# Performance work log

Hardware: AMD Instinct MI355X
Metric: run time of the kernel (lower is better)

## Reference

```python
import jax, jax.numpy as jnp
import numpy as np

EPS = 1e-5

def _conv2d(x, w, b, pad):
    # NCHW conv, stride 1
    out = jax.lax.conv_general_dilated(x, w, (1, 1), [(pad, pad), (pad, pad)],
                                       dimension_numbers=('NCHW', 'OIHW', 'NCHW'))
    return out + b[None, :, None, None]

def _deform_conv2d(x, offset, mask, weight, bias, pad):
    # torchvision.ops.deform_conv2d (modulated, stride=1, dilation=1)
    B, C, H, W = x.shape
    O, _, K, _ = weight.shape
    kk = K * K
    off = offset.reshape(B, kk, 2, H, W)
    dy, dx = off[:, :, 0], off[:, :, 1]          # [B,kk,H,W]
    ki = (jnp.arange(kk) // K).astype(x.dtype)
    kj = (jnp.arange(kk) % K).astype(x.dtype)
    hh = jnp.arange(H, dtype=x.dtype)
    ww = jnp.arange(W, dtype=x.dtype)
    ys = dy + (hh[None, :, None] + ki[:, None, None] - pad)[None]  # [B,kk,H,W]
    xs = dx + (ww[None, None, :] + kj[:, None, None] - pad)[None]
    y0 = jnp.floor(ys); x0 = jnp.floor(xs)
    wy = ys - y0; wx = xs - x0
    xf = x.reshape(B, C, H * W)

    def gather(yi, xi):
        valid = ((yi >= 0) & (yi <= H - 1) & (xi >= 0) & (xi <= W - 1)).astype(x.dtype)
        yc = jnp.clip(yi, 0, H - 1).astype(jnp.int32)
        xc = jnp.clip(xi, 0, W - 1).astype(jnp.int32)
        idx = (yc * W + xc).reshape(B, -1)
        v = jax.vmap(lambda f, i: f[:, i])(xf, idx).reshape(B, C, kk, H, W)
        return v * valid[:, None]

    one = jnp.asarray(1.0, x.dtype)
    sampled = (gather(y0, x0) * ((one - wy) * (one - wx))[:, None]
               + gather(y0, x0 + 1) * ((one - wy) * wx)[:, None]
               + gather(y0 + 1, x0) * (wy * (one - wx))[:, None]
               + gather(y0 + 1, x0 + 1) * (wy * wx)[:, None])
    sampled = sampled * mask[:, None]            # modulation
    out = jnp.einsum('bckhw,ock->bohw', sampled, weight.reshape(O, C, kk))
    return out + bias[None, :, None, None]

def setup_inputs() -> dict:
    key = jax.random.key(0)
    ks = jax.random.split(key, 7)
    B, C, H, W = 8, 768, 32, 32
    x = jax.random.normal(ks[0], (B, C, H, W), jnp.float32)
    proj_w = jax.random.normal(ks[1], (768, 768, 3, 3), jnp.float32) * 0.02
    proj_b = jax.random.normal(ks[2], (768,), jnp.float32) * 0.02
    offset_w = jax.random.normal(ks[3], (18, 768, 3, 3), jnp.float32) * 0.01
    offset_b = jax.random.normal(ks[4], (18,), jnp.float32) * 0.01
    mask_w = jax.random.normal(ks[5], (9, 768, 3, 3), jnp.float32) * 0.01
    mask_b = jax.random.normal(ks[6], (9,), jnp.float32) * 0.01
    gamma = jnp.ones((768,), jnp.float32)
    beta = jnp.zeros((768,), jnp.float32)
    return {"x": x, "proj_w": proj_w, "proj_b": proj_b, "offset_w": offset_w,
            "offset_b": offset_b, "mask_w": mask_w, "mask_b": mask_b,
            "gamma": gamma, "beta": beta}

def reference(x, proj_w, proj_b, offset_w, offset_b, mask_w, mask_b, gamma, beta):
    pad = 1
    H, W = x.shape[-2], x.shape[-1]
    max_off = float(min(H, W) // 4)
    offset = jnp.clip(_conv2d(x, offset_w, offset_b, pad), -max_off, max_off)
    mask = 2.0 * jax.nn.sigmoid(_conv2d(x, mask_w, mask_b, pad))
    y = _deform_conv2d(x, offset, mask, proj_w, proj_b, pad)
    # SyncBatchNorm (training-mode batch statistics, biased var)
    mean = jnp.mean(y, axis=(0, 2, 3))
    var = jnp.var(y, axis=(0, 2, 3))
    yn = (y - mean[None, :, None, None]) * jax.lax.rsqrt(var + EPS)[None, :, None, None]
    yn = yn * gamma[None, :, None, None] + beta[None, :, None, None]
    return x + jax.nn.gelu(yn, approximate=False)
```

## Files before the change

### kernel.cpp

```cpp
#include <hip/hip_runtime.h>
#include <math.h>

typedef __attribute__((ext_vector_type(4))) float f32x4;
typedef __attribute__((ext_vector_type(8))) short s16x8;
typedef __attribute__((ext_vector_type(4))) unsigned int u32x4;
typedef unsigned short ushort_t;

#define HW   1024
#define C_IN 768
#define B_N  8

__device__ inline ushort_t f2bf(float f) {
    unsigned u = __builtin_bit_cast(unsigned, f);
    unsigned r = u + 0x7FFFu + ((u >> 16) & 1u);
    return (ushort_t)(r >> 16);
}
__device__ inline float bf2f(short s) {
    return __builtin_bit_cast(float, ((unsigned)(ushort_t)s) << 16);
}
__device__ inline void glds16(const void* g, void* l) {
    __builtin_amdgcn_global_load_lds(
        (const __attribute__((address_space(1))) unsigned*)g,
        (__attribute__((address_space(3))) unsigned*)l, 16, 0, 0);
}

__global__ __launch_bounds__(256) void prepack_xt(
    const float* __restrict__ x, ushort_t* __restrict__ xt)
{
    __shared__ ushort_t tile[64][66];
    int bid = blockIdx.x;
    int b  = bid / 192;
    int r  = bid % 192;
    int cg = r / 16, pg = r % 16;
    int c0 = cg * 64, p0 = pg * 64;
    int t = threadIdx.x;
#pragma unroll
    for (int i = 0; i < 16; ++i) {
        int idx = t + i * 256;
        int cr = idx >> 6, col = idx & 63;
        tile[cr][col] = f2bf(x[(((size_t)b * C_IN + c0 + cr) << 10) + p0 + col]);
    }
    __syncthreads();
#pragma unroll
    for (int i = 0; i < 16; ++i) {
        int idx = t + i * 256;
        int pr = idx >> 6, col = idx & 63;
        xt[((size_t)(b << 10) + p0 + pr) * C_IN + c0 + col] = tile[col][pr];
    }
}

__global__ __launch_bounds__(256) void prepack_proj(
    const float* __restrict__ pw, ushort_t* __restrict__ A)
{
    __shared__ ushort_t tile[16][584];
    int bid = blockIdx.x;
    int mf = bid / 12, cblk = bid - mf * 12;
    int t = threadIdx.x;
    const float* src = pw + (size_t)mf * 16 * 6912 + cblk * 576;
#pragma unroll
    for (int i = 0; i < 36; ++i) {
        int f = i * 256 + t;
        int orow = f / 576, col = f - orow * 576;
        tile[orow][col] = f2bf(src[(size_t)orow * 6912 + col]);
    }
    __syncthreads();
    int lane = t & 63, fi0 = t >> 6;
    for (int it = 0; it < 5; ++it) {
        int fidx = it * 4 + fi0;
        if (fidx < 18) {
            int tap = fidx >> 1, half = fidx & 1;
            int s = tap * 24 + cblk * 2 + half;
            int cl0 = half * 32 + ((lane >> 4) << 3);
            s16x8 pk;
#pragma unroll
            for (int e = 0; e < 8; ++e)
                pk[e] = (short)tile[lane & 15][(cl0 + e) * 9 + tap];
            *(s16x8*)(A + ((size_t)(s * 48 + mf) * 64 + lane) * 8) = pk;
        }
    }
}

__global__ __launch_bounds__(256) void prepack_om(
    const float* __restrict__ offw, const float* __restrict__ mskw,
    ushort_t* __restrict__ A2)
{
    int t = blockIdx.x * 256 + threadIdx.x;
    int lane = t & 63;
    int smi  = t >> 6;
    int s  = smi >> 1, mf = smi & 1;
    int oc = mf * 16 + (lane & 15);
    int k0 = s * 32 + ((lane >> 4) << 3);
    int tap = k0 / 768;
    int c   = k0 - tap * 768;
    s16x8 pk;
#pragma unroll
    for (int e = 0; e < 8; ++e) pk[e] = 0;
    if (oc < 27) {
        const float* src = (oc < 18)
            ? offw + ((size_t)oc        * 768 + c) * 9 + tap
            : mskw + ((size_t)(oc - 18) * 768 + c) * 9 + tap;
#pragma unroll
        for (int e = 0; e < 8; ++e) pk[e] = (short)f2bf(src[e * 9]);
    }
    *(s16x8*)(A2 + (size_t)smi * 512 + lane * 8) = pk;
}

__global__ __launch_bounds__(256) void offmask_mfma(
    const ushort_t* __restrict__ xt, const ushort_t* __restrict__ A2,
    const float* __restrict__ offb, const float* __restrict__ mbias,
    float* __restrict__ offs, float* __restrict__ maskb)
{
    int bid = blockIdx.x;
    int b = bid >> 5, pt = bid & 31;
    int p0 = pt << 5;
    int t = threadIdx.x, lane = t & 63, wv = t >> 6;
    int mf = wv >> 1, nf = wv & 1;
    int q = lane >> 4;
    int px = p0 + nf * 16 + (lane & 15);
    int h = px >> 5, w = px & 31;
    const char* xb = (const char*)xt + (size_t)b * (HW * 1536);
    f32x4 acc = (f32x4){0.f, 0.f, 0.f, 0.f};

    for (int tap = 0; tap < 9; ++tap) {
        int yy = h + tap / 3 - 1, xx = w + tap % 3 - 1;
        bool ok = (yy >= 0 && yy < 32 && xx >= 0 && xx < 32);
        int pos = ok ? (yy * 32 + xx) : 0;
        const char* bp = xb + (size_t)pos * 1536 + q * 16;
        for (int cs = 0; cs < 24; ++cs) {
            int s = tap * 24 + cs;
            s16x8 bf;
            if (ok) bf = *(const s16x8*)(bp + cs * 64);
            else    bf = (s16x8){0, 0, 0, 0, 0, 0, 0, 0};
            s16x8 af = *(const s16x8*)(A2 + ((size_t)(s * 2 + mf) * 64 + lane) * 8);
            acc = __builtin_amdgcn_mfma_f32_16x16x32_bf16(af, bf, acc, 0, 0, 0);
        }
    }
#pragma unroll
    for (int r = 0; r < 4; ++r) {
        int oc = mf * 16 + ((lane >> 4) << 2) + r;
        if (oc < 18) {
            float v = acc[r] + offb[oc];
            v = fminf(fmaxf(v, -8.f), 8.f);
            offs[((b * 18 + oc) << 10) + px] = v;
        } else if (oc < 27) {
            float v = acc[r] + mbias[oc - 18];
            maskb[((b * 9 + oc - 18) << 10) + px] = 2.f / (1.f + expf(-v));
        }
    }
}

__global__ __launch_bounds__(512) void sample_pack(
    const ushort_t* __restrict__ xt,
    const float* __restrict__ offs, const float* __restrict__ maskb,
    ushort_t* __restrict__ Bp)
{
    __shared__ float4 mw[9][16];
    __shared__ int4   mi[9][16];
    int bid = blockIdx.x;
    int b = bid >> 6, pxg = bid & 63;
    int px0 = pxg << 4;
    int t = threadIdx.x;

    if (t < 144) {
        int tap = t >> 4, pxl = t & 15;
        int px = px0 + pxl, h = px >> 5, w = px & 31;
        float dy = offs[((b * 18 + 2 * tap) << 10) + px];
        float dx = offs[((b * 18 + 2 * tap + 1) << 10) + px];
        float m  = maskb[((b * 9 + tap) << 10) + px];
        float ys = dy + (float)(h + tap / 3 - 1);
        float xs = dx + (float)(w + tap % 3 - 1);
        float fy = floorf(ys), fx = floorf(xs);
        float wy = ys - fy, wx = xs - fx;
        int iy0 = (int)fy, ix0 = (int)fx;
        int iy1 = iy0 + 1, ix1 = ix0 + 1;
        float vy0 = (iy0 >= 0 && iy0 < 32) ? 1.f : 0.f;
        float vy1 = (iy1 >= 0 && iy1 < 32) ? 1.f : 0.f;
        float vx0 = (ix0 >= 0 && ix0 < 32) ? 1.f : 0.f;
        float vx1 = (ix1 >= 0 && ix1 < 32) ? 1.f : 0.f;
        int cy0 = min(max(iy0, 0), 31), cx0 = min(max(ix0, 0), 31);
        int cy1 = min(max(iy1, 0), 31), cx1 = min(max(ix1, 0), 31);
        float4 wv4;
        wv4.x = (1.f - wy) * (1.f - wx) * m * vy0 * vx0;
        wv4.y = (1.f - wy) * wx         * m * vy0 * vx1;
        wv4.z = wy         * (1.f - wx) * m * vy1 * vx0;
        wv4.w = wy         * wx         * m * vy1 * vx1;
        mw[tap][pxl] = wv4;
        mi[tap][pxl] = make_int4((cy0 * 32 + cx0) * 1536, (cy0 * 32 + cx1) * 1536,
                                 (cy1 * 32 + cx0) * 1536, (cy1 * 32 + cx1) * 1536);
    }
    __syncthreads();

    int lane = t & 63, wv = t >> 6;
    int pxl = lane & 15, ko = lane >> 4;
    const char* xb = (const char*)xt + (size_t)b * (HW * 1536);

    for (int s = wv; s < 216; s += 8) {
        int tap = s / 24, cq = s - tap * 24;
        float4 w4 = mw[tap][pxl];
        int4  i4 = mi[tap][pxl];
        const char* base = xb + cq * 64 + ko * 16;
        s16x8 g0 = *(const s16x8*)(base + i4.x);
        s16x8 g1 = *(const s16x8*)(base + i4.y);
        s16x8 g2 = *(const s16x8*)(base + i4.z);
        s16x8 g3 = *(const s16x8*)(base + i4.w);
        u32x4 bw;
#pragma unroll
        for (int e2 = 0; e2 < 4; ++e2) {
            float v0 = w4.x * bf2f(g0[2 * e2])     + w4.y * bf2f(g1[2 * e2])
                     + w4.z * bf2f(g2[2 * e2])     + w4.w * bf2f(g3[2 * e2]);
            float v1 = w4.x * bf2f(g0[2 * e2 + 1]) + w4.y * bf2f(g1[2 * e2 + 1])
                     + w4.z * bf2f(g2[2 * e2 + 1]) + w4.w * bf2f(g3[2 * e2 + 1]);
            unsigned rr;
            asm("v_cvt_pk_bf16_f32 %0, %1, %2" : "=v"(rr) : "v"(v0), "v"(v1));
            bw[e2] = rr;
        }
        *(u32x4*)(Bp + ((size_t)(s * 8 + b) * 64 + pxg) * 512 + lane * 8) = bw;
    }
}

__global__ __launch_bounds__(512, 4) void deform_gemm_lds(
    const ushort_t* __restrict__ Amat, const ushort_t* __restrict__ Bp,
    float* __restrict__ y)
{
    __shared__ __align__(16) char Sbuf[2][32768];

    int id = blockIdx.x;
    int b = id & 7;
    int pxt = (id >> 3) & 15;
    int otile = id >> 7;
    int p0 = pxt << 6;
    int t = threadIdx.x, lane = t & 63, wv = t >> 6;
    int wm = wv >> 1, wn = wv & 1;

    f32x4 acc[3][2];
#pragma unroll
    for (int f = 0; f < 3; ++f)
#pragma unroll
        for (int n = 0; n < 2; ++n) acc[f][n] = (f32x4){0.f, 0.f, 0.f, 0.f};

#define STAGE(BUF, P) do {                                                  \
    int s0_ = 2 * (P);                                                      \
    _Pragma("unroll")                                                       \
    for (int i_ = 0; i_ < 4; ++i_) {                                        \
        int c_ = wv * 4 + i_;                                               \
        const char* src_;                                                   \
        if (c_ < 24) {                                                      \
            int kk_ = c_ / 12, f_ = c_ - kk_ * 12;                          \
            src_ = (const char*)Amat +                                      \
                (((size_t)(s0_ + kk_) * 48 + otile * 12 + f_) << 10);       \
        } else {                                                            \
            int d_ = c_ - 24; int kk_ = d_ >> 2, pg_ = d_ & 3;              \
            src_ = (const char*)Bp +                                        \
                (((size_t)((s0_ + kk_) * 8 + b) * 64 + pxt * 4 + pg_) << 10); \
        }                                                                   \
        glds16(src_ + lane * 16, &Sbuf[BUF][c_ << 10]);                     \
    }                                                                       \
} while (0)

#define MFMA_PHASE(BUF) do {                                                \
    _Pragma("unroll")                                                       \
    for (int kk_ = 0; kk_ < 2; ++kk_) {                                     \
        const char* ab_ = &Sbuf[BUF][(kk_ * 12 + wm * 3) << 10] + lane * 16; \
        s16x8 a0_ = *(const s16x8*)(ab_);                                   \
        s16x8 a1_ = *(const s16x8*)(ab_ + 1024);                            \
        s16x8 a2_ = *(const s16x8*)(ab_ + 2048);                            \
        const char* bb_ = &Sbuf[BUF][(24 + kk_ * 4 + wn * 2) << 10] + lane * 16; \
        s16x8 b0_ = *(const s16x8*)(bb_);                                   \
        s16x8 b1_ = *(const s16x8*)(bb_ + 1024);                            \
        acc[0][0] = __builtin_amdgcn_mfma_f32_16x16x32_bf16(a0_, b0_, acc[0][0], 0, 0, 0); \
        acc[0][1] = __builtin_amdgcn_mfma_f32_16x16x32_bf16(a0_, b1_, acc[0][1], 0, 0, 0); \
        acc[1][0] = __builtin_amdgcn_mfma_f32_16x16x32_bf16(a1_, b0_, acc[1][0], 0, 0, 0); \
        acc[1][1] = __builtin_amdgcn_mfma_f32_16x16x32_bf16(a1_, b1_, acc[1][1], 0, 0, 0); \
        acc[2][0] = __builtin_amdgcn_mfma_f32_16x16x32_bf16(a2_, b0_, acc[2][0], 0, 0, 0); \
        acc[2][1] = __builtin_amdgcn_mfma_f32_16x16x32_bf16(a2_, b1_, acc[2][1], 0, 0, 0); \
    }                                                                       \
} while (0)

    STAGE(0, 0);
    asm volatile("s_waitcnt vmcnt(0)" ::: "memory");
    __builtin_amdgcn_s_barrier();

    for (int p = 0; p < 108; ++p) {
        int buf = p & 1;
        if (p + 1 < 108) STAGE(buf ^ 1, p + 1);
        __builtin_amdgcn_s_setprio(1);
        MFMA_PHASE(buf);
        __builtin_amdgcn_s_setprio(0);
        asm volatile("s_waitcnt vmcnt(0) lgkmcnt(0)" ::: "memory");
        __builtin_amdgcn_s_barrier();
    }

    int pxo = p0 + wn * 32 + (lane & 15);
    int obase = otile * 192 + wm * 48;
#pragma unroll
    for (int f = 0; f < 3; ++f) {
        int orow = obase + f * 16 + ((lane >> 4) << 2);
#pragma unroll
        for (int r = 0; r < 4; ++r) {
            size_t rowoff = ((size_t)(b * 768 + orow + r) << 10);
            y[rowoff + pxo]      = acc[f][0][r];
            y[rowoff + pxo + 16] = acc[f][1][r];
        }
    }
#undef STAGE
#undef MFMA_PHASE
}

__global__ __launch_bounds__(512, 4) void deform_mfma_fused(
    const ushort_t* __restrict__ xt, const ushort_t* __restrict__ Amat,
    const float* __restrict__ offs, const float* __restrict__ maskb,
    float* __restrict__ y)
{
    __shared__ float4 meta_w[576];
    __shared__ int4   meta_i[576];
    __shared__ __align__(16) ushort_t Bs[2][64][64];

    int id = blockIdx.x;
    int b = id & 7;
    int pxt = (id >> 3) & 15;
    int otile = id >> 7;
    int p0 = pxt << 6;
    int t = threadIdx.x, lane = t & 63, wv = t >> 6;
    int wm = wv >> 1, wn = wv & 1;
    int q4 = lane >> 4;

    int bpx = wv * 8 + (lane >> 3);
    int oct = lane & 7;
    const int wchunk = (oct ^ (bpx & 7)) * 8;

    for (int i = t; i < 576; i += 512) {
        int k = i >> 6, j = i & 63;
        int hw = p0 + j, h = hw >> 5, w = hw & 31;
        float dy = offs[((b * 18 + 2 * k) << 10) + hw];
        float dx = offs[((b * 18 + 2 * k + 1) << 10) + hw];
        float m  = maskb[((b * 9 + k) << 10) + hw];
        float ys = dy + (float)(h + k / 3 - 1);
        float xs = dx + (float)(w + k % 3 - 1);
        float fy = floorf(ys), fx = floorf(xs);
        float wy = ys - fy, wx = xs - fx;
        int iy0 = (int)fy, ix0 = (int)fx;
        int iy1 = iy0 + 1, ix1 = ix0 + 1;
        float vy0 = (iy0 >= 0 && iy0 < 32) ? 1.f : 0.f;
        float vy1 = (iy1 >= 0 && iy1 < 32) ? 1.f : 0.f;
        float vx0 = (ix0 >= 0 && ix0 < 32) ? 1.f : 0.f;
        float vx1 = (ix1 >= 0 && ix1 < 32) ? 1.f : 0.f;
        int cy0 = min(max(iy0, 0), 31), cx0 = min(max(ix0, 0), 31);
        int cy1 = min(max(iy1, 0), 31), cx1 = min(max(ix1, 0), 31);
        float4 wv4;
        wv4.x = (1.f - wy) * (1.f - wx) * m * vy0 * vx0;
        wv4.y = (1.f - wy) * wx         * m * vy0 * vx1;
        wv4.z = wy         * (1.f - wx) * m * vy1 * vx0;
        wv4.w = wy         * wx         * m * vy1 * vx1;
        meta_w[i] = wv4;
        meta_i[i] = make_int4((cy0 * 32 + cx0) * 1536, (cy0 * 32 + cx1) * 1536,
                              (cy1 * 32 + cx0) * 1536, (cy1 * 32 + cx1) * 1536);
    }
    asm volatile("s_waitcnt lgkmcnt(0)" ::: "memory");
    __builtin_amdgcn_s_barrier();

    f32x4 acc[3][2];
#pragma unroll
    for (int f = 0; f < 3; ++f)
#pragma unroll
        for (int n = 0; n < 2; ++n) acc[f][n] = (f32x4){0.f, 0.f, 0.f, 0.f};

    const char* xb = (const char*)xt + (size_t)b * (HW * 1536);
    const int afrag0 = otile * 12 + wm * 3;

    s16x8 ga0, ga1, ga2, ga3, gb0, gb1, gb2, gb3;
    float4 w4a, w4b;

#define WBAR() do { asm volatile("s_waitcnt lgkmcnt(0)" ::: "memory"); \
                    __builtin_amdgcn_s_barrier(); } while (0)
#define ISSUE(G0, G1, G2, G3, W4, qq) do {                                  \
    int nt_ = (qq) / 12, nc_ = (qq) - nt_ * 12;                             \
    W4 = meta_w[nt_ * 64 + bpx];                                            \
    int4 i4_ = meta_i[nt_ * 64 + bpx];                                      \
    const char* bsrc_ = xb + nc_ * 128 + oct * 16;                          \
    G0 = *(const s16x8*)(bsrc_ + i4_.x);                                    \
    G1 = *(const s16x8*)(bsrc_ + i4_.y);                                    \
    G2 = *(const s16x8*)(bsrc_ + i4_.z);                                    \
    G3 = *(const s16x8*)(bsrc_ + i4_.w);                                    \
} while (0)
#define BUILD(G0, G1, G2, G3, W4, BUF) do {                                 \
    u32x4 bw_;                                                              \
    _Pragma("unroll")                                                       \
    for (int e2 = 0; e2 < 4; ++e2) {                                        \
        float v0_ = W4.x * bf2f(G0[2*e2])   + W4.y * bf2f(G1[2*e2])         \
                  + W4.z * bf2f(G2[2*e2])   + W4.w * bf2f(G3[2*e2]);        \
        float v1_ = W4.x * bf2f(G0[2*e2+1]) + W4.y * bf2f(G1[2*e2+1])       \
                  + W4.z * bf2f(G2[2*e2+1]) + W4.w * bf2f(G3[2*e2+1]);      \
        unsigned rr_;                                                       \
        asm("v_cvt_pk_bf16_f32 %0, %1, %2" : "=v"(rr_) : "v"(v0_), "v"(v1_)); \
        bw_[e2] = rr_;                                                      \
    }                                                                       \
    *(u32x4*)&Bs[BUF][bpx][wchunk] = bw_;                                   \
} while (0)
#define MFMA_PHASE_F(P, BUF) do {                                           \
    _Pragma("unroll")                                                       \
    for (int kk = 0; kk < 2; ++kk) {                                        \
        int s_ = 2 * (P) + kk;                                              \
        const s16x8* ap_ = (const s16x8*)(Amat +                            \
            ((size_t)(s_ * 48 + afrag0) * 64 + lane) * 8);                  \
        s16x8 a0_ = ap_[0], a1_ = ap_[64], a2_ = ap_[128];                  \
        int rc_ = ((kk * 4 + q4) ^ (lane & 7)) * 8;                         \
        s16x8 b0_ = *(const s16x8*)&Bs[BUF][wn * 32 + (lane & 15)][rc_];    \
        s16x8 b1_ = *(const s16x8*)&Bs[BUF][wn * 32 + 16 + (lane & 15)][rc_]; \
        acc[0][0] = __builtin_amdgcn_mfma_f32_16x16x32_bf16(a0_, b0_, acc[0][0], 0, 0, 0); \
        acc[0][1] = __builtin_amdgcn_mfma_f32_16x16x32_bf16(a0_, b1_, acc[0][1], 0, 0, 0); \
        acc[1][0] = __builtin_amdgcn_mfma_f32_16x16x32_bf16(a1_, b0_, acc[1][0], 0, 0, 0); \
        acc[1][1] = __builtin_amdgcn_mfma_f32_16x16x32_bf16(a1_, b1_, acc[1][1], 0, 0, 0); \
        acc[2][0] = __builtin_amdgcn_mfma_f32_16x16x32_bf16(a2_, b0_, acc[2][0], 0, 0, 0); \
        acc[2][1] = __builtin_amdgcn_mfma_f32_16x16x32_bf16(a2_, b1_, acc[2][1], 0, 0, 0); \
    }                                                                       \
} while (0)

    ISSUE(ga0, ga1, ga2, ga3, w4a, 0);
    ISSUE(gb0, gb1, gb2, gb3, w4b, 1);
    BUILD(ga0, ga1, ga2, ga3, w4a, 0);
    WBAR();
    for (int pp = 0; pp < 54; ++pp) {
        int pe = 2 * pp;
        if (pp < 53) ISSUE(ga0, ga1, ga2, ga3, w4a, pe + 2);
        MFMA_PHASE_F(pe, 0);
        BUILD(gb0, gb1, gb2, gb3, w4b, 1);
        WBAR();
        int po = pe + 1;
        if (pp < 53) ISSUE(gb0, gb1, gb2, gb3, w4b, po + 2);
        MFMA_PHASE_F(po, 1);
        if (pp < 53) BUILD(ga0, ga1, ga2, ga3, w4a, 0);
        WBAR();
    }
    int pxo = p0 + wn * 32 + (lane & 15);
    int obase = otile * 192 + wm * 48;
#pragma unroll
    for (int f = 0; f < 3; ++f) {
        int orow = obase + f * 16 + ((lane >> 4) << 2);
#pragma unroll
        for (int r = 0; r < 4; ++r) {
            size_t rowoff = ((size_t)(b * 768 + orow + r) << 10);
            y[rowoff + pxo]      = acc[f][0][r];
            y[rowoff + pxo + 16] = acc[f][1][r];
        }
    }
#undef WBAR
#undef ISSUE
#undef BUILD
#undef MFMA_PHASE_F
}

__global__ __launch_bounds__(256) void stats_kernel(
    const float* __restrict__ y, float* __restrict__ stats)
{
    int o = blockIdx.x;
    int tid = threadIdx.x;
    float s1 = 0.f, s2 = 0.f;
    for (int i = tid; i < B_N * HW; i += 256) {
        int b = i >> 10, hw = i & 1023;
        float v = y[(((size_t)b * 768 + o) << 10) + hw];
        s1 += v; s2 += v * v;
    }
#pragma unroll
    for (int off = 32; off > 0; off >>= 1) {
        s1 += __shfl_down(s1, off);
        s2 += __shfl_down(s2, off);
    }
    __shared__ float ls1[4], ls2[4];
    int wid = tid >> 6, lane = tid & 63;
    if (lane == 0) { ls1[wid] = s1; ls2[wid] = s2; }
    __syncthreads();
    if (tid == 0) {
        float t1 = ls1[0] + ls1[1] + ls1[2] + ls1[3];
        float t2 = ls2[0] + ls2[1] + ls2[2] + ls2[3];
        float mean = t1 * (1.0f / 8192.0f);
        float var  = t2 * (1.0f / 8192.0f) - mean * mean;
        stats[o]       = mean;
        stats[768 + o] = 1.0f / sqrtf(var + 1e-5f);
    }
}

__global__ __launch_bounds__(256) void finalize_kernel(
    const float* __restrict__ x, const float* __restrict__ stats,
    const float* __restrict__ gamma, const float* __restrict__ beta,
    float* __restrict__ y)
{
    const int total4 = B_N * 768 * HW / 4;
    for (int f = blockIdx.x * 256 + threadIdx.x; f < total4;
         f += gridDim.x * 256) {
        int e = f << 2;
        int o = (e >> 10) % 768;
        float mean = stats[o], rstd = stats[768 + o];
        float ga = gamma[o], be = beta[o];
        float4 v  = ((const float4*)y)[f];
        float4 xv = ((const float4*)x)[f];
        float4 r;
        {
            float yn = (v.x - mean) * rstd * ga + be;
            r.x = xv.x + 0.5f * yn * (1.0f + erff(yn * 0.70710678f));
        }
        {
            float yn = (v.y - mean) * rstd * ga + be;
            r.y = xv.y + 0.5f * yn * (1.0f + erff(yn * 0.70710678f));
        }
        {
            float yn = (v.z - mean) * rstd * ga + be;
            r.z = xv.z + 0.5f * yn * (1.0f + erff(yn * 0.70710678f));
        }
        {
            float yn = (v.w - mean) * rstd * ga + be;
            r.w = xv.w + 0.5f * yn * (1.0f + erff(yn * 0.70710678f));
        }
        ((float4*)y)[f] = r;
    }
}

extern "C" void kernel_launch(void* const* d_in, const int* in_sizes, int n_in,
                              void* d_out, int out_size, void* d_ws, size_t ws_size,
                              hipStream_t stream)
{
    const float* x        = (const float*)d_in[0];
    const float* proj_w   = (const float*)d_in[1];
    const float* offset_w = (const float*)d_in[3];
    const float* offset_b = (const float*)d_in[4];
    const float* mask_w   = (const float*)d_in[5];
    const float* mask_b   = (const float*)d_in[6];
    const float* gamma    = (const float*)d_in[7];
    const float* beta     = (const float*)d_in[8];

    char* ws = (char*)d_ws;
    float*    offs  = (float*)(ws);
    float*    maskb = (float*)(ws + 589824);
    float*    stats = (float*)(ws + 884736);
    ushort_t* A     = (ushort_t*)(ws + 890880);
    ushort_t* A2    = (ushort_t*)(ws + 11507712);
    ushort_t* xt    = (ushort_t*)(ws + 11950080);
    ushort_t* Bp    = (ushort_t*)(ws + 24532992);
    float* y = (float*)d_out;

    const size_t NEED_SPLIT = 24532992ull + 113246208ull;

    prepack_xt<<<1536, 256, 0, stream>>>(x, xt);
    prepack_om<<<108, 256, 0, stream>>>(offset_w, mask_w, A2);
    prepack_proj<<<576, 256, 0, stream>>>(proj_w, A);
    offmask_mfma<<<256, 256, 0, stream>>>(xt, A2, offset_b, mask_b, offs, maskb);

    if (ws_size >= NEED_SPLIT) {
        sample_pack<<<512, 512, 0, stream>>>(xt, offs, maskb, Bp);
        deform_gemm_lds<<<512, 512, 0, stream>>>(A, Bp, y);
    } else {
        deform_mfma_fused<<<512, 512, 0, stream>>>(xt, A, offs, maskb, y);
    }

    stats_kernel<<<768, 256, 0, stream>>>(y, stats);
    finalize_kernel<<<2048, 256, 0, stream>>>(x, stats, gamma, beta, y);
}
```

Measured before the change: 252.8 us.

## Widen GEMM tile to 128 pixels with 4-stage LDS pipeline and 1024-thread blocks

Replaces the 512-thread double-buffered deformable GEMM with a 1024-thread kernel that covers 192 outputs × 128 pixels per block. It cuts the K-step per stage to one slice and uses a 4-deep LDS ring, issuing loads two stages ahead. Partial vmcnt waits replace the full drain, and there is one barrier per step. The aim is to raise A-tile reuse and hide global-to-LDS latency better, at the cost of fewer blocks (256) and tight ring-buffer reuse that relies on correct wait counts.

```diff
diff --git a/kernel.cpp b/kernel.cpp
--- a/kernel.cpp
+++ b/kernel.cpp
@@ -218,19 +218,18 @@
     }
 }
 
-__global__ __launch_bounds__(512, 4) void deform_gemm_lds(
+__global__ __launch_bounds__(1024, 2) void deform_gemm_lds2(
     const ushort_t* __restrict__ Amat, const ushort_t* __restrict__ Bp,
     float* __restrict__ y)
 {
-    __shared__ __align__(16) char Sbuf[2][32768];
+    __shared__ __align__(16) char Sbuf[4][20480];
 
     int id = blockIdx.x;
     int b = id & 7;
-    int pxt = (id >> 3) & 15;
-    int otile = id >> 7;
-    int p0 = pxt << 6;
+    int pxt = (id >> 3) & 7;
+    int otile = id >> 6;
     int t = threadIdx.x, lane = t & 63, wv = t >> 6;
-    int wm = wv >> 1, wn = wv & 1;
+    int wm = wv >> 2, wn = wv & 3;
 
     f32x4 acc[3][2];
 #pragma unroll
@@ -238,59 +237,57 @@
 #pragma unroll
         for (int n = 0; n < 2; ++n) acc[f][n] = (f32x4){0.f, 0.f, 0.f, 0.f};
 
-#define STAGE(BUF, P) do {                                                  \
-    int s0_ = 2 * (P);                                                      \
-    _Pragma("unroll")                                                       \
-    for (int i_ = 0; i_ < 4; ++i_) {                                        \
-        int c_ = wv * 4 + i_;                                               \
-        const char* src_;                                                   \
-        if (c_ < 24) {                                                      \
-            int kk_ = c_ / 12, f_ = c_ - kk_ * 12;                          \
-            src_ = (const char*)Amat +                                      \
-                (((size_t)(s0_ + kk_) * 48 + otile * 12 + f_) << 10);       \
-        } else {                                                            \
-            int d_ = c_ - 24; int kk_ = d_ >> 2, pg_ = d_ & 3;              \
-            src_ = (const char*)Bp +                                        \
-                (((size_t)((s0_ + kk_) * 8 + b) * 64 + pxt * 4 + pg_) << 10); \
-        }                                                                   \
-        glds16(src_ + lane * 16, &Sbuf[BUF][c_ << 10]);                     \
-    }                                                                       \
+#define CHUNK_SRC(c_, s_) ((c_) < 12                                         \
+    ? (const char*)Amat + (((size_t)(s_) * 48 + otile * 12 + (c_)) << 10)    \
+    : (const char*)Bp + ((((size_t)(s_) * 8 + b) * 64 + pxt * 8 + ((c_) - 12)) << 10))
+
+#define STAGE(BUF, s_) do {                                                  \
+    int c1_ = wv;                                                            \
+    glds16(CHUNK_SRC(c1_, s_) + lane * 16, &Sbuf[BUF][c1_ << 10]);           \
+    if (wv < 4) {                                                            \
+        int c2_ = 16 + wv;                                                   \
+        glds16(CHUNK_SRC(c2_, s_) + lane * 16, &Sbuf[BUF][c2_ << 10]);       \
+    }                                                                        \
 } while (0)
 
-#define MFMA_PHASE(BUF) do {                                                \
-    _Pragma("unroll")                                                       \
-    for (int kk_ = 0; kk_ < 2; ++kk_) {                                     \
-        const char* ab_ = &Sbuf[BUF][(kk_ * 12 + wm * 3) << 10] + lane * 16; \
-        s16x8 a0_ = *(const s16x8*)(ab_);                                   \
-        s16x8 a1_ = *(const s16x8*)(ab_ + 1024);                            \
-        s16x8 a2_ = *(const s16x8*)(ab_ + 2048);                            \
-        const char* bb_ = &Sbuf[BUF][(24 + kk_ * 4 + wn * 2) << 10] + lane * 16; \
-        s16x8 b0_ = *(const s16x8*)(bb_);                                   \
-        s16x8 b1_ = *(const s16x8*)(bb_ + 1024);                            \
-        acc[0][0] = __builtin_amdgcn_mfma_f32_16x16x32_bf16(a0_, b0_, acc[0][0], 0, 0, 0); \
-        acc[0][1] = __builtin_amdgcn_mfma_f32_16x16x32_bf16(a0_, b1_, acc[0][1], 0, 0, 0); \
-        acc[1][0] = __builtin_amdgcn_mfma_f32_16x16x32_bf16(a1_, b0_, acc[1][0], 0, 0, 0); \
-        acc[1][1] = __builtin_amdgcn_mfma_f32_16x16x32_bf16(a1_, b1_, acc[1][1], 0, 0, 0); \
-        acc[2][0] = __builtin_amdgcn_mfma_f32_16x16x32_bf16(a2_, b0_, acc[2][0], 0, 0, 0); \
-        acc[2][1] = __builtin_amdgcn_mfma_f32_16x16x32_bf16(a2_, b1_, acc[2][1], 0, 0, 0); \
-    }                                                                       \
+#define MFMA_PHASE(BUF) do {                                                 \
+    const char* ab_ = &Sbuf[BUF][(wm * 3) << 10] + lane * 16;                \
+    s16x8 a0_ = *(const s16x8*)(ab_);                                        \
+    s16x8 a1_ = *(const s16x8*)(ab_ + 1024);                                 \
+    s16x8 a2_ = *(const s16x8*)(ab_ + 2048);                                 \
+    const char* bb_ = &Sbuf[BUF][(12 + wn * 2) << 10] + lane * 16;           \
+    s16x8 b0_ = *(const s16x8*)(bb_);                                        \
+    s16x8 b1_ = *(const s16x8*)(bb_ + 1024);                                 \
+    acc[0][0] = __builtin_amdgcn_mfma_f32_16x16x32_bf16(a0_, b0_, acc[0][0], 0, 0, 0); \
+    acc[0][1] = __builtin_amdgcn_mfma_f32_16x16x32_bf16(a0_, b1_, acc[0][1], 0, 0, 0); \
+    acc[1][0] = __builtin_amdgcn_mfma_f32_16x16x32_bf16(a1_, b0_, acc[1][0], 0, 0, 0); \
+    acc[1][1] = __builtin_amdgcn_mfma_f32_16x16x32_bf16(a1_, b1_, acc[1][1], 0, 0, 0); \
+    acc[2][0] = __builtin_amdgcn_mfma_f32_16x16x32_bf16(a2_, b0_, acc[2][0], 0, 0, 0); \
+    acc[2][1] = __builtin_amdgcn_mfma_f32_16x16x32_bf16(a2_, b1_, acc[2][1], 0, 0, 0); \
 } while (0)
 
     STAGE(0, 0);
+    STAGE(1, 1);
+
+    for (int p = 0; p < 214; ++p) {
+        int bufc = p & 3;
+        STAGE((p + 2) & 3, p + 2);
+        if (wv < 4) asm volatile("s_waitcnt vmcnt(4)" ::: "memory");
+        else        asm volatile("s_waitcnt vmcnt(2)" ::: "memory");
+        __builtin_amdgcn_s_barrier();
+        __builtin_amdgcn_s_setprio(1);
+        MFMA_PHASE(bufc);
+        __builtin_amdgcn_s_setprio(0);
+    }
+    if (wv < 4) asm volatile("s_waitcnt vmcnt(2)" ::: "memory");
+    else        asm volatile("s_waitcnt vmcnt(1)" ::: "memory");
+    __builtin_amdgcn_s_barrier();
+    MFMA_PHASE(214 & 3);
     asm volatile("s_waitcnt vmcnt(0)" ::: "memory");
     __builtin_amdgcn_s_barrier();
-
-    for (int p = 0; p < 108; ++p) {
-        int buf = p & 1;
-        if (p + 1 < 108) STAGE(buf ^ 1, p + 1);
-        __builtin_amdgcn_s_setprio(1);
-        MFMA_PHASE(buf);
-        __builtin_amdgcn_s_setprio(0);
-        asm volatile("s_waitcnt vmcnt(0) lgkmcnt(0)" ::: "memory");
-        __builtin_amdgcn_s_barrier();
-    }
-
-    int pxo = p0 + wn * 32 + (lane & 15);
+    MFMA_PHASE(215 & 3);
+
+    int pxo = pxt * 128 + wn * 32 + (lane & 15);
     int obase = otile * 192 + wm * 48;
 #pragma unroll
     for (int f = 0; f < 3; ++f) {
@@ -302,6 +299,7 @@
             y[rowoff + pxo + 16] = acc[f][1][r];
         }
     }
+#undef CHUNK_SRC
 #undef STAGE
 #undef MFMA_PHASE
 }
@@ -546,7 +544,7 @@
 
     if (ws_size >= NEED_SPLIT) {
         sample_pack<<<512, 512, 0, stream>>>(xt, offs, maskb, Bp);
-        deform_gemm_lds<<<512, 512, 0, stream>>>(A, Bp, y);
+        deform_gemm_lds2<<<256, 1024, 0, stream>>>(A, Bp, y);
     } else {
         deform_mfma_fused<<<512, 512, 0, stream>>>(xt, A, offs, maskb, y);
     }
```

Measured after the change: 255.8 us. About the same (+1.2%).

## Split GEMM staging into A double-buffer and B triple-buffer with partial waits

Applied to the files above, without the earlier changes.

The deform GEMM kernel now keeps separate LDS buffers for weight tiles (double-buffered) and sampled-column tiles (triple-buffered). B loads are issued two stages ahead and waits use partial vmcnt counts instead of draining all loads each iteration, so global-to-LDS copies overlap MFMA work more deeply. The sample_pack block index mapping is also reordered so that adjacent blocks cover different batches. The explicit prologue/epilogue and vmcnt counts add complexity and risk of ordering mistakes, and the third B buffer increases LDS use.

```diff
diff --git a/kernel.cpp b/kernel.cpp
--- a/kernel.cpp
+++ b/kernel.cpp
@@ -157,7 +157,7 @@
     __shared__ float4 mw[9][16];
     __shared__ int4   mi[9][16];
     int bid = blockIdx.x;
-    int b = bid >> 6, pxg = bid & 63;
+    int b = bid & 7, pxg = bid >> 3;
     int px0 = pxg << 4;
     int t = threadIdx.x;
 
@@ -218,11 +218,12 @@
     }
 }
 
-__global__ __launch_bounds__(512, 4) void deform_gemm_lds(
+__global__ __launch_bounds__(512, 4) void deform_gemm_lds3(
     const ushort_t* __restrict__ Amat, const ushort_t* __restrict__ Bp,
     float* __restrict__ y)
 {
-    __shared__ __align__(16) char Sbuf[2][32768];
+    __shared__ __align__(16) char Abuf[2][24576];
+    __shared__ __align__(16) char Bbuf[3][8192];
 
     int id = blockIdx.x;
     int b = id & 7;
@@ -238,33 +239,32 @@
 #pragma unroll
         for (int n = 0; n < 2; ++n) acc[f][n] = (f32x4){0.f, 0.f, 0.f, 0.f};
 
-#define STAGE(BUF, P) do {                                                  \
-    int s0_ = 2 * (P);                                                      \
+#define STAGE_A(BUF, s_) do {                                               \
     _Pragma("unroll")                                                       \
-    for (int i_ = 0; i_ < 4; ++i_) {                                        \
-        int c_ = wv * 4 + i_;                                               \
-        const char* src_;                                                   \
-        if (c_ < 24) {                                                      \
-            int kk_ = c_ / 12, f_ = c_ - kk_ * 12;                          \
-            src_ = (const char*)Amat +                                      \
-                (((size_t)(s0_ + kk_) * 48 + otile * 12 + f_) << 10);       \
-        } else {                                                            \
-            int d_ = c_ - 24; int kk_ = d_ >> 2, pg_ = d_ & 3;              \
-            src_ = (const char*)Bp +                                        \
-                (((size_t)((s0_ + kk_) * 8 + b) * 64 + pxt * 4 + pg_) << 10); \
-        }                                                                   \
-        glds16(src_ + lane * 16, &Sbuf[BUF][c_ << 10]);                     \
+    for (int i_ = 0; i_ < 3; ++i_) {                                        \
+        int c_ = wv * 3 + i_;                                               \
+        int kk_ = c_ / 12, f_ = c_ - kk_ * 12;                              \
+        const char* src_ = (const char*)Amat +                              \
+            (((size_t)(2 * (s_) + kk_) * 48 + otile * 12 + f_) << 10);      \
+        glds16(src_ + lane * 16, &Abuf[BUF][c_ << 10]);                     \
     }                                                                       \
 } while (0)
 
-#define MFMA_PHASE(BUF) do {                                                \
+#define STAGE_B(BUF, s_) do {                                               \
+    int kk_ = wv >> 2, pg_ = wv & 3;                                        \
+    const char* src_ = (const char*)Bp +                                    \
+        ((((size_t)(2 * (s_) + kk_) * 8 + b) * 64 + pxt * 4 + pg_) << 10);  \
+    glds16(src_ + lane * 16, &Bbuf[BUF][wv << 10]);                         \
+} while (0)
+
+#define MFMA_PHASE(AB, BB) do {                                             \
     _Pragma("unroll")                                                       \
     for (int kk_ = 0; kk_ < 2; ++kk_) {                                     \
-        const char* ab_ = &Sbuf[BUF][(kk_ * 12 + wm * 3) << 10] + lane * 16; \
+        const char* ab_ = &Abuf[AB][(kk_ * 12 + wm * 3) << 10] + lane * 16; \
         s16x8 a0_ = *(const s16x8*)(ab_);                                   \
         s16x8 a1_ = *(const s16x8*)(ab_ + 1024);                            \
         s16x8 a2_ = *(const s16x8*)(ab_ + 2048);                            \
-        const char* bb_ = &Sbuf[BUF][(24 + kk_ * 4 + wn * 2) << 10] + lane * 16; \
+        const char* bb_ = &Bbuf[BB][(kk_ * 4 + wn * 2) << 10] + lane * 16;  \
         s16x8 b0_ = *(const s16x8*)(bb_);                                   \
         s16x8 b1_ = *(const s16x8*)(bb_ + 1024);                            \
         acc[0][0] = __builtin_amdgcn_mfma_f32_16x16x32_bf16(a0_, b0_, acc[0][0], 0, 0, 0); \
@@ -276,19 +276,32 @@
     }                                                                       \
 } while (0)
 
-    STAGE(0, 0);
+    STAGE_A(0, 0);
+    STAGE_B(0, 0);
+    STAGE_B(1, 1);
+
+    int bb = 0;
+    for (int p = 0; p < 106; ++p) {
+        STAGE_A((p + 1) & 1, p + 1);
+        int bn = bb + 2; if (bn >= 3) bn -= 3;
+        STAGE_B(bn, p + 2);
+        asm volatile("s_waitcnt vmcnt(5)" ::: "memory");
+        __builtin_amdgcn_s_barrier();
+        __builtin_amdgcn_s_setprio(1);
+        MFMA_PHASE(p & 1, bb);
+        __builtin_amdgcn_s_setprio(0);
+        __builtin_amdgcn_s_barrier();
+        ++bb; if (bb == 3) bb = 0;
+    }
+    STAGE_A(1, 107);
+    asm volatile("s_waitcnt vmcnt(4)" ::: "memory");
+    __builtin_amdgcn_s_barrier();
+    MFMA_PHASE(0, bb);
+    __builtin_amdgcn_s_barrier();
+    ++bb; if (bb == 3) bb = 0;
     asm volatile("s_waitcnt vmcnt(0)" ::: "memory");
     __builtin_amdgcn_s_barrier();
-
-    for (int p = 0; p < 108; ++p) {
-        int buf = p & 1;
-        if (p + 1 < 108) STAGE(buf ^ 1, p + 1);
-        __builtin_amdgcn_s_setprio(1);
-        MFMA_PHASE(buf);
-        __builtin_amdgcn_s_setprio(0);
-        asm volatile("s_waitcnt vmcnt(0) lgkmcnt(0)" ::: "memory");
-        __builtin_amdgcn_s_barrier();
-    }
+    MFMA_PHASE(1, bb);
 
     int pxo = p0 + wn * 32 + (lane & 15);
     int obase = otile * 192 + wm * 48;
@@ -302,7 +315,8 @@
             y[rowoff + pxo + 16] = acc[f][1][r];
         }
     }
-#undef STAGE
+#undef STAGE_A
+#undef STAGE_B
 #undef MFMA_PHASE
 }
 
@@ -546,7 +560,7 @@
 
     if (ws_size >= NEED_SPLIT) {
         sample_pack<<<512, 512, 0, stream>>>(xt, offs, maskb, Bp);
-        deform_gemm_lds<<<512, 512, 0, stream>>>(A, Bp, y);
+        deform_gemm_lds3<<<512, 512, 0, stream>>>(A, Bp, y);
     } else {
         deform_mfma_fused<<<512, 512, 0, stream>>>(xt, A, offs, maskb, y);
     }
```

Result: no change. 255.2 us (+0.9%).

## Fuse BN statistics into deform GEMM epilogue and split-K the offset/mask conv

Applied to the files above, without the earlier changes.

The deform GEMM epilogue now reduces per-channel sum and sum-of-squares with wave shuffles and atomically adds them into a zeroed stats buffer. This removes the separate stats kernel, which reread the whole output, on the split path. The finalize kernel now derives mean and rstd from the raw sums. The offset/mask conv kernel splits its K loop over four wave groups in 1024-thread blocks with an LDS reduction, giving it more parallelism. sample_pack block indexing is also reordered so consecutive blocks cover different batches. Atomics add contention and make the sums order-dependent.

```diff
diff --git a/kernel.cpp b/kernel.cpp
--- a/kernel.cpp
+++ b/kernel.cpp
@@ -105,46 +105,55 @@
     *(s16x8*)(A2 + (size_t)smi * 512 + lane * 8) = pk;
 }
 
-__global__ __launch_bounds__(256) void offmask_mfma(
+__global__ __launch_bounds__(1024) void offmask_mfma(
     const ushort_t* __restrict__ xt, const ushort_t* __restrict__ A2,
     const float* __restrict__ offb, const float* __restrict__ mbias,
     float* __restrict__ offs, float* __restrict__ maskb)
 {
+    __shared__ f32x4 red[16][64];
     int bid = blockIdx.x;
     int b = bid >> 5, pt = bid & 31;
     int p0 = pt << 5;
     int t = threadIdx.x, lane = t & 63, wv = t >> 6;
-    int mf = wv >> 1, nf = wv & 1;
+    int kq = wv >> 2, quad = wv & 3;
+    int mf = quad >> 1, nf = quad & 1;
     int q = lane >> 4;
     int px = p0 + nf * 16 + (lane & 15);
     int h = px >> 5, w = px & 31;
     const char* xb = (const char*)xt + (size_t)b * (HW * 1536);
     f32x4 acc = (f32x4){0.f, 0.f, 0.f, 0.f};
 
-    for (int tap = 0; tap < 9; ++tap) {
+    int s0 = kq * 54;
+    for (int s = s0; s < s0 + 54; ++s) {
+        int tap = s / 24, cs = s - tap * 24;
         int yy = h + tap / 3 - 1, xx = w + tap % 3 - 1;
         bool ok = (yy >= 0 && yy < 32 && xx >= 0 && xx < 32);
         int pos = ok ? (yy * 32 + xx) : 0;
-        const char* bp = xb + (size_t)pos * 1536 + q * 16;
-        for (int cs = 0; cs < 24; ++cs) {
-            int s = tap * 24 + cs;
-            s16x8 bf;
-            if (ok) bf = *(const s16x8*)(bp + cs * 64);
-            else    bf = (s16x8){0, 0, 0, 0, 0, 0, 0, 0};
-            s16x8 af = *(const s16x8*)(A2 + ((size_t)(s * 2 + mf) * 64 + lane) * 8);
-            acc = __builtin_amdgcn_mfma_f32_16x16x32_bf16(af, bf, acc, 0, 0, 0);
-        }
-    }
-#pragma unroll
-    for (int r = 0; r < 4; ++r) {
-        int oc = mf * 16 + ((lane >> 4) << 2) + r;
-        if (oc < 18) {
-            float v = acc[r] + offb[oc];
-            v = fminf(fmaxf(v, -8.f), 8.f);
-            offs[((b * 18 + oc) << 10) + px] = v;
-        } else if (oc < 27) {
-            float v = acc[r] + mbias[oc - 18];
-            maskb[((b * 9 + oc - 18) << 10) + px] = 2.f / (1.f + expf(-v));
+        const char* bp = xb + (size_t)pos * 1536 + cs * 64 + q * 16;
+        s16x8 bf;
+        if (ok) bf = *(const s16x8*)bp;
+        else    bf = (s16x8){0, 0, 0, 0, 0, 0, 0, 0};
+        s16x8 af = *(const s16x8*)(A2 + ((size_t)(s * 2 + mf) * 64 + lane) * 8);
+        acc = __builtin_amdgcn_mfma_f32_16x16x32_bf16(af, bf, acc, 0, 0, 0);
+    }
+    red[wv][lane] = acc;
+    __syncthreads();
+    if (wv < 4) {
+        f32x4 r1 = red[wv + 4][lane];
+        f32x4 r2 = red[wv + 8][lane];
+        f32x4 r3 = red[wv + 12][lane];
+        acc += r1; acc += r2; acc += r3;
+#pragma unroll
+        for (int r = 0; r < 4; ++r) {
+            int oc = mf * 16 + ((lane >> 4) << 2) + r;
+            if (oc < 18) {
+                float v = acc[r] + offb[oc];
+                v = fminf(fmaxf(v, -8.f), 8.f);
+                offs[((b * 18 + oc) << 10) + px] = v;
+            } else if (oc < 27) {
+                float v = acc[r] + mbias[oc - 18];
+                maskb[((b * 9 + oc - 18) << 10) + px] = 2.f / (1.f + expf(-v));
+            }
         }
     }
 }
@@ -157,7 +166,7 @@
     __shared__ float4 mw[9][16];
     __shared__ int4   mi[9][16];
     int bid = blockIdx.x;
-    int b = bid >> 6, pxg = bid & 63;
+    int b = bid & 7, pxg = bid >> 3;
     int px0 = pxg << 4;
     int t = threadIdx.x;
 
@@ -220,7 +229,7 @@
 
 __global__ __launch_bounds__(512, 4) void deform_gemm_lds(
     const ushort_t* __restrict__ Amat, const ushort_t* __restrict__ Bp,
-    float* __restrict__ y)
+    float* __restrict__ y, float* __restrict__ stats)
 {
     __shared__ __align__(16) char Sbuf[2][32768];
 
@@ -297,9 +306,21 @@
         int orow = obase + f * 16 + ((lane >> 4) << 2);
 #pragma unroll
         for (int r = 0; r < 4; ++r) {
+            float a = acc[f][0][r], c = acc[f][1][r];
             size_t rowoff = ((size_t)(b * 768 + orow + r) << 10);
-            y[rowoff + pxo]      = acc[f][0][r];
-            y[rowoff + pxo + 16] = acc[f][1][r];
+            y[rowoff + pxo]      = a;
+            y[rowoff + pxo + 16] = c;
+            float s1 = a + c;
+            float s2 = a * a + c * c;
+#pragma unroll
+            for (int m = 1; m < 16; m <<= 1) {
+                s1 += __shfl_xor(s1, m);
+                s2 += __shfl_xor(s2, m);
+            }
+            if ((lane & 15) == 0) {
+                atomicAdd(&stats[orow + r], s1);
+                atomicAdd(&stats[768 + orow + r], s2);
+            }
         }
     }
 #undef STAGE
@@ -470,12 +491,8 @@
     if (lane == 0) { ls1[wid] = s1; ls2[wid] = s2; }
     __syncthreads();
     if (tid == 0) {
-        float t1 = ls1[0] + ls1[1] + ls1[2] + ls1[3];
-        float t2 = ls2[0] + ls2[1] + ls2[2] + ls2[3];
-        float mean = t1 * (1.0f / 8192.0f);
-        float var  = t2 * (1.0f / 8192.0f) - mean * mean;
-        stats[o]       = mean;
-        stats[768 + o] = 1.0f / sqrtf(var + 1e-5f);
+        stats[o]       = ls1[0] + ls1[1] + ls1[2] + ls1[3];
+        stats[768 + o] = ls2[0] + ls2[1] + ls2[2] + ls2[3];
     }
 }
 
@@ -489,7 +506,10 @@
          f += gridDim.x * 256) {
         int e = f << 2;
         int o = (e >> 10) % 768;
-        float mean = stats[o], rstd = stats[768 + o];
+        float s1 = stats[o], s2 = stats[768 + o];
+        float mean = s1 * (1.0f / 8192.0f);
+        float var  = s2 * (1.0f / 8192.0f) - mean * mean;
+        float rstd = 1.0f / sqrtf(var + 1e-5f);
         float ga = gamma[o], be = beta[o];
         float4 v  = ((const float4*)y)[f];
         float4 xv = ((const float4*)x)[f];
@@ -542,15 +562,16 @@
     prepack_xt<<<1536, 256, 0, stream>>>(x, xt);
     prepack_om<<<108, 256, 0, stream>>>(offset_w, mask_w, A2);
     prepack_proj<<<576, 256, 0, stream>>>(proj_w, A);
-    offmask_mfma<<<256, 256, 0, stream>>>(xt, A2, offset_b, mask_b, offs, maskb);
+    offmask_mfma<<<256, 1024, 0, stream>>>(xt, A2, offset_b, mask_b, offs, maskb);
 
     if (ws_size >= NEED_SPLIT) {
+        hipMemsetAsync(stats, 0, 1536 * sizeof(float), stream);
         sample_pack<<<512, 512, 0, stream>>>(xt, offs, maskb, Bp);
-        deform_gemm_lds<<<512, 512, 0, stream>>>(A, Bp, y);
+        deform_gemm_lds<<<512, 512, 0, stream>>>(A, Bp, y, stats);
     } else {
         deform_mfma_fused<<<512, 512, 0, stream>>>(xt, A, offs, maskb, y);
-    }
-
-    stats_kernel<<<768, 256, 0, stream>>>(y, stats);
+        stats_kernel<<<768, 256, 0, stream>>>(y, stats);
+    }
+
     finalize_kernel<<<2048, 256, 0, stream>>>(x, stats, gamma, beta, y);
 }
```

Result: no change. 253.5 us (+0.3%).
